# Kernel optimization log

Hardware: AMD Instinct MI355X
Metric: run time of the kernel (lower is better)

Reference implementation:

```python
import jax, jax.numpy as jnp
import numpy as np

BN_EPS = 1e-3
NUM_HEADS = 4
HEAD_CH = 16  # embed_channels // num_heads = 64 // 4


def _conv_bn(x, w, g, b, rm, rv, pad):
    # Conv2d (no bias) followed by eval-mode BatchNorm2d, activation=Identity.
    y = jax.lax.conv_general_dilated(
        x, w, window_strides=(1, 1), padding=[(pad, pad), (pad, pad)],
        dimension_numbers=("NCHW", "OIHW", "NCHW"))
    s = g * jax.lax.rsqrt(rv + BN_EPS)
    return y * s[None, :, None, None] + (b - rm * s)[None, :, None, None]


def setup_inputs() -> dict:
    key = jax.random.key(0)
    ks = jax.random.split(key, 16)
    B, Cin, H, W = 8, 128, 160, 160
    N, Cg, Ce, Co = 80, 512, 64, 128
    x = jax.random.normal(ks[0], (B, Cin, H, W), jnp.float32)
    guide = jax.random.normal(ks[1], (B, N, Cg), jnp.float32)
    # embed_conv (1x1) + BN params
    w_embed = jax.random.normal(ks[2], (Ce, Cin, 1, 1), jnp.float32) * 0.05
    g1 = jnp.ones((Ce,), jnp.float32)
    b1 = jnp.zeros((Ce,), jnp.float32)
    rm1 = jax.random.normal(ks[3], (Ce,), jnp.float32) * 0.1
    rv1 = jax.random.uniform(ks[4], (Ce,), jnp.float32) + 0.5
    # guide_fc
    Wg = jax.random.normal(ks[5], (Ce, Cg), jnp.float32) * 0.02
    bg = jnp.zeros((Ce,), jnp.float32)
    # per-head bias
    attn_bias = jnp.zeros((NUM_HEADS,), jnp.float32)
    # project_conv (3x3) + BN params
    w_proj = jax.random.normal(ks[6], (Co, Cin, 3, 3), jnp.float32) * 0.02
    g2 = jnp.ones((Co,), jnp.float32)
    b2 = jnp.zeros((Co,), jnp.float32)
    rm2 = jax.random.normal(ks[7], (Co,), jnp.float32) * 0.1
    rv2 = jax.random.uniform(ks[8], (Co,), jnp.float32) + 0.5
    return {"x": x, "guide": guide, "w_embed": w_embed, "g1": g1, "b1": b1,
            "rm1": rm1, "rv1": rv1, "Wg": Wg, "bg": bg, "attn_bias": attn_bias,
            "w_proj": w_proj, "g2": g2, "b2": b2, "rm2": rm2, "rv2": rv2}


def reference(x, guide, w_embed, g1, b1, rm1, rv1, Wg, bg, attn_bias,
              w_proj, g2, b2, rm2, rv2):
    B, _, H, W = x.shape
    nh, hc = NUM_HEADS, HEAD_CH
    # guide_fc -> [B, N, nh, hc]
    g = (jnp.einsum("bnc,ec->bne", guide, Wg) + bg).reshape(B, -1, nh, hc)
    # embed_conv (1x1, BN, no act) -> [B, nh, hc, H, W]
    e = _conv_bn(x, w_embed, g1, b1, rm1, rv1, 0).reshape(B, nh, hc, H, W)
    # attn: dot over head channels, max over N guides, scale, bias, sigmoid
    aw = jnp.einsum("bmchw,bnmc->bmhwn", e, g)  # [B, nh, H, W, N]
    aw = jnp.max(aw, axis=-1) * (1.0 / np.sqrt(hc)) + attn_bias[None, :, None, None]
    aw = jax.nn.sigmoid(aw)  # scale == 1.0 (with_scale=False)
    # project_conv (3x3, BN, no act), gate per-head, merge heads
    xp = _conv_bn(x, w_proj, g2, b2, rm2, rv2, 1).reshape(B, nh, -1, H, W)
    return (xp * aw[:, :, None]).reshape(B, -1, H, W)
```

## Files before the change

kernel.cpp:

```cpp
#include <hip/hip_runtime.h>
#include <hip/hip_bf16.h>
#include <stdint.h>


typedef __attribute__((ext_vector_type(8))) short short8;
typedef __attribute__((ext_vector_type(4))) float f32x4;

#define PCH2 ((size_t)8 * 162 * 176 * 32)

__device__ __forceinline__ unsigned short f2bf(float f) {
  unsigned int u = __float_as_uint(f);
  u += 0x7fff + ((u >> 16) & 1);
  return (unsigned short)(u >> 16);
}

__device__ __forceinline__ short8 zero8() {
  short8 z = {0,0,0,0,0,0,0,0};
  return z;
}

__global__ __launch_bounds__(192) void k_prep_x(const float* __restrict__ x,
                                                unsigned short* __restrict__ P2) {
  int b = blockIdx.x / 162, hp = blockIdx.x % 162;
  int wp = threadIdx.x;
  if (wp >= 176) return;
  size_t pix = (((size_t)b * 162 + hp) * 176 + wp) * 32;
  bool interior = (hp >= 1) && (hp <= 160) && (wp >= 8) && (wp < 168);
  if (!interior) {
#pragma unroll
    for (int cs = 0; cs < 4; ++cs)
#pragma unroll
      for (int s = 0; s < 4; ++s)
        *(short8*)(&P2[(size_t)cs * PCH2 + pix + s * 8]) = zero8();
    return;
  }
  int h = hp - 1, w = wp - 8;
  const float* xb = x + (size_t)b * 128 * 25600 + h * 160 + w;
  for (int cs = 0; cs < 4; ++cs) {
#pragma unroll
    for (int s = 0; s < 4; ++s) {
      short8 v;
#pragma unroll
      for (int j = 0; j < 8; ++j) {
        float f = xb[(size_t)(cs * 32 + s * 8 + j) * 25600];
        v[j] = (short)f2bf(f);
      }
      *(short8*)(&P2[(size_t)cs * PCH2 + pix + s * 8]) = v;
    }
  }
}

__global__ __launch_bounds__(256) void k_prep_misc(
    const float* __restrict__ w_embed, const float* __restrict__ w_proj,
    const float* __restrict__ g2, const float* __restrict__ b2,
    const float* __restrict__ rm2, const float* __restrict__ rv2,
    unsigned short* __restrict__ W1t, unsigned short* __restrict__ Wpt,
    float* __restrict__ s2, float* __restrict__ t2) {
  int idx = blockIdx.x * 256 + threadIdx.x;
  if (idx < 8192) { W1t[idx] = f2bf(w_embed[idx]); return; }
  idx -= 8192;
  if (idx < 147456) {
    int cs = idx / 36864, r = idx - cs * 36864;
    int tap = r >> 12, r2 = r & 4095;
    int co = r2 >> 5, ci5 = r2 & 31;
    int ci = cs * 32 + ci5;
    Wpt[idx] = f2bf(w_proj[(co * 128 + ci) * 9 + tap]);
    return;
  }
  idx -= 147456;
  if (idx < 128) {
    float s = g2[idx] * rsqrtf(rv2[idx] + 1e-3f);
    s2[idx] = s;
    t2[idx] = b2[idx] - rm2[idx] * s;
  }
}

__global__ __launch_bounds__(64) void k_guide(
    const float* __restrict__ guide, const float* __restrict__ Wg,
    const float* __restrict__ bg, const float* __restrict__ g1,
    const float* __restrict__ b1, const float* __restrict__ rm1,
    const float* __restrict__ rv1, unsigned short* __restrict__ Gpad,
    float* __restrict__ Cst) {
  int b = blockIdx.x / 80, n = blockIdx.x % 80;
  __shared__ float gs[512];
  const float* gr = guide + ((size_t)b * 80 + n) * 512;
  for (int i = threadIdx.x; i < 512; i += 64) gs[i] = gr[i];
  __syncthreads();
  int ce = threadIdx.x;
  const float* wr = Wg + (size_t)ce * 512;
  float acc = 0.f;
  for (int k = 0; k < 512; k += 4)
    acc += gs[k] * wr[k] + gs[k + 1] * wr[k + 1] + gs[k + 2] * wr[k + 2] +
           gs[k + 3] * wr[k + 3];
  float raw = acc + bg[ce];
  float s1 = g1[ce] * rsqrtf(rv1[ce] + 1e-3f);
  float t1 = b1[ce] - rm1[ce] * s1;
  int head = ce >> 4, c = ce & 15;
  size_t gp = (((size_t)b * 4 + head) * 80 + n) * 32;
  Gpad[gp + c] = f2bf(raw * s1);
  Gpad[gp + 16 + c] = 0;
  float cp = raw * t1;
  cp += __shfl_xor(cp, 1);
  cp += __shfl_xor(cp, 2);
  cp += __shfl_xor(cp, 4);
  cp += __shfl_xor(cp, 8);
  if (c == 0) Cst[((size_t)b * 4 + head) * 80 + n] = cp;
}

__global__ __launch_bounds__(256, 4) void k_attn(
    const unsigned short* __restrict__ P2, const unsigned short* __restrict__ W1t,
    const unsigned short* __restrict__ Gpad, const float* __restrict__ Cst,
    const float* __restrict__ attn_bias, float* __restrict__ aw) {
  __shared__ unsigned short E[16384];
  int b = blockIdx.x & 7;
  int px0 = (blockIdx.x >> 3) * 256;
  int tid = threadIdx.x, lane = tid & 63, wv = tid >> 6;
  int l15 = lane & 15, l4 = lane >> 4;

  f32x4 acc[4][4];
#pragma unroll
  for (int mt = 0; mt < 4; ++mt)
#pragma unroll
    for (int nt = 0; nt < 4; ++nt) acc[mt][nt] = (f32x4){0.f, 0.f, 0.f, 0.f};

  size_t Ab[4];
#pragma unroll
  for (int mt = 0; mt < 4; ++mt) {
    int px = px0 + wv * 64 + mt * 16 + l15;
    int h = px / 160, w = px - h * 160;
    Ab[mt] = (((size_t)b * 162 + h + 1) * 176 + (w + 8)) * 32;
  }
#pragma unroll
  for (int kc = 0; kc < 4; ++kc) {
    short8 A[4], Bf[4];
#pragma unroll
    for (int mt = 0; mt < 4; ++mt)
      A[mt] = *(const short8*)(P2 + (size_t)kc * PCH2 + Ab[mt] + l4 * 8);
#pragma unroll
    for (int nt = 0; nt < 4; ++nt)
      Bf[nt] = *(const short8*)(W1t + (nt * 16 + l15) * 128 + kc * 32 + l4 * 8);
#pragma unroll
    for (int mt = 0; mt < 4; ++mt)
#pragma unroll
      for (int nt = 0; nt < 4; ++nt)
        acc[mt][nt] = __builtin_amdgcn_mfma_f32_16x16x32_bf16(A[mt], Bf[nt],
                                                              acc[mt][nt], 0, 0, 0);
  }
#pragma unroll
  for (int mt = 0; mt < 4; ++mt)
#pragma unroll
    for (int nt = 0; nt < 4; ++nt)
#pragma unroll
      for (int r = 0; r < 4; ++r) {
        int pxl = wv * 64 + mt * 16 + l4 * 4 + r;
        int slot = (nt * 2 + (l15 >> 3)) ^ (pxl & 7);
        E[pxl * 64 + slot * 8 + (l15 & 7)] = f2bf(acc[mt][nt][r]);
      }
  __syncthreads();

  const f32x4 zf = (f32x4){0.f, 0.f, 0.f, 0.f};
#pragma unroll
  for (int head = 0; head < 4; ++head) {
    short8 Ga[5];
    f32x4 cst[5];
#pragma unroll
    for (int m5 = 0; m5 < 5; ++m5) {
      Ga[m5] = *(const short8*)(Gpad + (((size_t)b * 4 + head) * 80 + m5 * 16 + l15) * 32 + l4 * 8);
      cst[m5] = *(const f32x4*)(Cst + ((size_t)b * 4 + head) * 80 + m5 * 16 + l4 * 4);
    }
    float bias = attn_bias[head];
#pragma unroll
    for (int nt = 0; nt < 4; ++nt) {
      int pxl = wv * 64 + nt * 16 + l15;
      int rslot = (head * 2 + (l4 & 1)) ^ (pxl & 7);
      short8 Bf = *(const short8*)(&E[pxl * 64 + rslot * 8]);
      float mx = -3.0e38f;
#pragma unroll
      for (int m5 = 0; m5 < 5; ++m5) {
        f32x4 s = __builtin_amdgcn_mfma_f32_16x16x32_bf16(Ga[m5], Bf, zf, 0, 0, 0);
#pragma unroll
        for (int r = 0; r < 4; ++r) mx = fmaxf(mx, s[r] + cst[m5][r]);
      }
      mx = fmaxf(mx, __shfl_xor(mx, 16));
      mx = fmaxf(mx, __shfl_xor(mx, 32));
      if (lane < 16) {
        float v = 1.f / (1.f + __expf(-(mx * 0.25f + bias)));
        aw[((size_t)b * 4 + head) * 25600 + px0 + wv * 64 + nt * 16 + lane] = v;
      }
    }
  }
}

__global__ __launch_bounds__(256, 3) void k_conv(
    const unsigned short* __restrict__ P2, const unsigned short* __restrict__ Wpt,
    const float* __restrict__ s2, const float* __restrict__ t2,
    const float* __restrict__ aw, float* __restrict__ out) {
  __shared__ unsigned short XA[2][7680];
  __shared__ unsigned short XB[2][4096];
  int b = blockIdx.x & 7, r2b = blockIdx.x >> 3;
  int ht = r2b / 5, wt = r2b % 5;
  int h0 = ht * 4, w0 = wt * 32;
  int tid = threadIdx.x, lane = tid & 63, wv = tid >> 6;
  int l15 = lane & 15, l4 = lane >> 4;
  int mh = wv >> 1, nh = wv & 1;

  size_t aoff[4];
  bool aval[4];
#pragma unroll
  for (int i = 0; i < 4; ++i) {
    int c = i * 256 + tid;
    aval[i] = (c < 960);
    int cc = aval[i] ? c : 0;
    int row = cc / 160, rem = cc - row * 160;
    int px = rem >> 2, sp = rem & 3;
    int s = sp ^ ((px >> 1) & 3);
    aoff[i] = (((size_t)b * 162 + h0 + row) * 176 + (w0 + 7 + px)) * 32 + s * 8;
  }
  int boff[2];
#pragma unroll
  for (int i = 0; i < 2; ++i) {
    int c = i * 256 + tid;
    int co = c >> 2, sp = c & 3;
    boff[i] = co * 32 + (sp ^ ((co >> 1) & 3)) * 8;
  }
  int abase[2][3];
#pragma unroll
  for (int wh = 0; wh < 2; ++wh)
#pragma unroll
    for (int kx = 0; kx < 3; ++kx) {
      int px = wh * 16 + l15 + kx;
      abase[wh][kx] = px * 4 + (l4 ^ ((px >> 1) & 3));
    }
  int bchunk[4];
#pragma unroll
  for (int nt = 0; nt < 4; ++nt) {
    int co = nh * 64 + nt * 16 + l15;
    bchunk[nt] = co * 4 + (l4 ^ ((co >> 1) & 3));
  }

  f32x4 acc[4][4];
#pragma unroll
  for (int j = 0; j < 4; ++j)
#pragma unroll
    for (int nt = 0; nt < 4; ++nt) acc[j][nt] = (f32x4){0.f, 0.f, 0.f, 0.f};

  short8 areg[4], breg[2];
#pragma unroll
  for (int i = 0; i < 4; ++i)
    if (aval[i]) areg[i] = *(const short8*)(P2 + aoff[i]);
#pragma unroll
  for (int i = 0; i < 2; ++i) breg[i] = *(const short8*)(Wpt + boff[i]);
#pragma unroll
  for (int i = 0; i < 4; ++i)
    if (aval[i]) *(short8*)(&XA[0][(i * 256 + tid) * 8]) = areg[i];
#pragma unroll
  for (int i = 0; i < 2; ++i) *(short8*)(&XB[0][(i * 256 + tid) * 8]) = breg[i];
  __syncthreads();

  for (int cs = 0; cs < 4; ++cs) {
#pragma unroll
    for (int tap = 0; tap < 9; ++tap) {
      int t = cs * 9 + tap;
      int ky = tap / 3, kx = tap - ky * 3;
      if (tap == 0 && cs < 3) {
#pragma unroll
        for (int i = 0; i < 4; ++i)
          if (aval[i]) areg[i] = *(const short8*)(P2 + (size_t)(cs + 1) * PCH2 + aoff[i]);
      }
      if (t < 35) {
#pragma unroll
        for (int i = 0; i < 2; ++i)
          breg[i] = *(const short8*)(Wpt + (size_t)(t + 1) * 4096 + boff[i]);
      }
      short8 A[4], Bf[4];
#pragma unroll
      for (int j = 0; j < 4; ++j) {
        int row = mh * 2 + (j >> 1) + ky;
        A[j] = *(const short8*)(&XA[cs & 1][(row * 160 + abase[j & 1][kx]) * 8]);
      }
#pragma unroll
      for (int nt = 0; nt < 4; ++nt)
        Bf[nt] = *(const short8*)(&XB[t & 1][bchunk[nt] * 8]);
#pragma unroll
      for (int j = 0; j < 4; ++j)
#pragma unroll
        for (int nt = 0; nt < 4; ++nt)
          acc[j][nt] = __builtin_amdgcn_mfma_f32_16x16x32_bf16(A[j], Bf[nt],
                                                               acc[j][nt], 0, 0, 0);
      if (t < 35) {
#pragma unroll
        for (int i = 0; i < 2; ++i)
          *(short8*)(&XB[(t + 1) & 1][(i * 256 + tid) * 8]) = breg[i];
      }
      if (tap == 8 && cs < 3) {
#pragma unroll
        for (int i = 0; i < 4; ++i)
          if (aval[i]) *(short8*)(&XA[(cs + 1) & 1][(i * 256 + tid) * 8]) = areg[i];
      }
      if (t < 35) __syncthreads();
    }
  }

  float s2v[4], t2v[4];
#pragma unroll
  for (int nt = 0; nt < 4; ++nt) {
    int co = nh * 64 + nt * 16 + l15;
    s2v[nt] = s2[co];
    t2v[nt] = t2[co];
  }
#pragma unroll
  for (int j = 0; j < 4; ++j) {
    int hl = mh * 2 + (j >> 1), wh = j & 1;
    int h = h0 + hl, wbase = w0 + wh * 16 + l4 * 4;
    f32x4 aw0 = *(const f32x4*)(aw + (size_t)(b * 4 + nh * 2) * 25600 + h * 160 + wbase);
    f32x4 aw1 = *(const f32x4*)(aw + (size_t)(b * 4 + nh * 2 + 1) * 25600 + h * 160 + wbase);
#pragma unroll
    for (int nt = 0; nt < 4; ++nt) {
      int co = nh * 64 + nt * 16 + l15;
      f32x4 g = (nt < 2) ? aw0 : aw1;
      f32x4 o;
#pragma unroll
      for (int r = 0; r < 4; ++r) o[r] = (acc[j][nt][r] * s2v[nt] + t2v[nt]) * g[r];
      *(f32x4*)(out + (size_t)(b * 128 + co) * 25600 + h * 160 + wbase) = o;
    }
  }
}

extern "C" void kernel_launch(void* const* d_in, const int* in_sizes, int n_in,
                              void* d_out, int out_size, void* d_ws, size_t ws_size,
                              hipStream_t stream) {
  (void)in_sizes; (void)n_in; (void)out_size; (void)ws_size;
  const float* x         = (const float*)d_in[0];
  const float* guide     = (const float*)d_in[1];
  const float* w_embed   = (const float*)d_in[2];
  const float* g1        = (const float*)d_in[3];
  const float* b1        = (const float*)d_in[4];
  const float* rm1       = (const float*)d_in[5];
  const float* rv1       = (const float*)d_in[6];
  const float* Wg        = (const float*)d_in[7];
  const float* bg        = (const float*)d_in[8];
  const float* attn_bias = (const float*)d_in[9];
  const float* w_proj    = (const float*)d_in[10];
  const float* g2        = (const float*)d_in[11];
  const float* b2        = (const float*)d_in[12];
  const float* rm2       = (const float*)d_in[13];
  const float* rv2       = (const float*)d_in[14];
  float* out = (float*)d_out;

  char* ws = (char*)d_ws;
  unsigned short* P2   = (unsigned short*)(ws);
  unsigned short* W1t  = (unsigned short*)(ws + 58392576);
  unsigned short* Wpt  = (unsigned short*)(ws + 58408960);
  unsigned short* Gpad = (unsigned short*)(ws + 58703872);
  float* Cst           = (float*)(ws + 58867712);
  float* s2            = (float*)(ws + 58877952);
  float* t2            = (float*)(ws + 58878464);
  float* aw            = (float*)(ws + 58878976);

  k_prep_x<<<8 * 162, 192, 0, stream>>>(x, P2);
  k_prep_misc<<<609, 256, 0, stream>>>(w_embed, w_proj, g2, b2, rm2, rv2, W1t, Wpt, s2, t2);
  k_guide<<<640, 64, 0, stream>>>(guide, Wg, bg, g1, b1, rm1, rv1, Gpad, Cst);
  k_attn<<<800, 256, 0, stream>>>(P2, W1t, Gpad, Cst, attn_bias, aw);
  k_conv<<<1600, 256, 0, stream>>>(P2, Wpt, s2, t2, aw, out);
}
```

Before: 165.8 us.

## Fuse attention-gate computation into the 3x3 conv kernel and register-buffer weights

Merges the separate attention kernel into the conv kernel. The 1x1 embed GEMM reuses the centre-tap A fragments already staged in LDS, the embeddings are written into the freed XA buffer, and the per-pixel sigmoid gate is computed and kept in shared memory, so the aw round trip through global memory and one launch are gone. Conv weights are now read straight from global memory into a 3-deep register ring instead of being staged through LDS, which removes the per-tap barriers. The cost is higher register pressure (launch bounds lowered to 2 waves per SIMD), more global weight traffic per block, and some leftover dead variables.

```diff
diff --git a/kernel.cpp b/kernel.cpp
--- a/kernel.cpp
+++ b/kernel.cpp
@@ -107,96 +107,14 @@
   if (c == 0) Cst[((size_t)b * 4 + head) * 80 + n] = cp;
 }
 
-__global__ __launch_bounds__(256, 4) void k_attn(
+__global__ __launch_bounds__(256, 2) void k_mega(
     const unsigned short* __restrict__ P2, const unsigned short* __restrict__ W1t,
-    const unsigned short* __restrict__ Gpad, const float* __restrict__ Cst,
-    const float* __restrict__ attn_bias, float* __restrict__ aw) {
-  __shared__ unsigned short E[16384];
-  int b = blockIdx.x & 7;
-  int px0 = (blockIdx.x >> 3) * 256;
-  int tid = threadIdx.x, lane = tid & 63, wv = tid >> 6;
-  int l15 = lane & 15, l4 = lane >> 4;
-
-  f32x4 acc[4][4];
-#pragma unroll
-  for (int mt = 0; mt < 4; ++mt)
-#pragma unroll
-    for (int nt = 0; nt < 4; ++nt) acc[mt][nt] = (f32x4){0.f, 0.f, 0.f, 0.f};
-
-  size_t Ab[4];
-#pragma unroll
-  for (int mt = 0; mt < 4; ++mt) {
-    int px = px0 + wv * 64 + mt * 16 + l15;
-    int h = px / 160, w = px - h * 160;
-    Ab[mt] = (((size_t)b * 162 + h + 1) * 176 + (w + 8)) * 32;
-  }
-#pragma unroll
-  for (int kc = 0; kc < 4; ++kc) {
-    short8 A[4], Bf[4];
-#pragma unroll
-    for (int mt = 0; mt < 4; ++mt)
-      A[mt] = *(const short8*)(P2 + (size_t)kc * PCH2 + Ab[mt] + l4 * 8);
-#pragma unroll
-    for (int nt = 0; nt < 4; ++nt)
-      Bf[nt] = *(const short8*)(W1t + (nt * 16 + l15) * 128 + kc * 32 + l4 * 8);
-#pragma unroll
-    for (int mt = 0; mt < 4; ++mt)
-#pragma unroll
-      for (int nt = 0; nt < 4; ++nt)
-        acc[mt][nt] = __builtin_amdgcn_mfma_f32_16x16x32_bf16(A[mt], Bf[nt],
-                                                              acc[mt][nt], 0, 0, 0);
-  }
-#pragma unroll
-  for (int mt = 0; mt < 4; ++mt)
-#pragma unroll
-    for (int nt = 0; nt < 4; ++nt)
-#pragma unroll
-      for (int r = 0; r < 4; ++r) {
-        int pxl = wv * 64 + mt * 16 + l4 * 4 + r;
-        int slot = (nt * 2 + (l15 >> 3)) ^ (pxl & 7);
-        E[pxl * 64 + slot * 8 + (l15 & 7)] = f2bf(acc[mt][nt][r]);
-      }
-  __syncthreads();
-
-  const f32x4 zf = (f32x4){0.f, 0.f, 0.f, 0.f};
-#pragma unroll
-  for (int head = 0; head < 4; ++head) {
-    short8 Ga[5];
-    f32x4 cst[5];
-#pragma unroll
-    for (int m5 = 0; m5 < 5; ++m5) {
-      Ga[m5] = *(const short8*)(Gpad + (((size_t)b * 4 + head) * 80 + m5 * 16 + l15) * 32 + l4 * 8);
-      cst[m5] = *(const f32x4*)(Cst + ((size_t)b * 4 + head) * 80 + m5 * 16 + l4 * 4);
-    }
-    float bias = attn_bias[head];
-#pragma unroll
-    for (int nt = 0; nt < 4; ++nt) {
-      int pxl = wv * 64 + nt * 16 + l15;
-      int rslot = (head * 2 + (l4 & 1)) ^ (pxl & 7);
-      short8 Bf = *(const short8*)(&E[pxl * 64 + rslot * 8]);
-      float mx = -3.0e38f;
-#pragma unroll
-      for (int m5 = 0; m5 < 5; ++m5) {
-        f32x4 s = __builtin_amdgcn_mfma_f32_16x16x32_bf16(Ga[m5], Bf, zf, 0, 0, 0);
-#pragma unroll
-        for (int r = 0; r < 4; ++r) mx = fmaxf(mx, s[r] + cst[m5][r]);
-      }
-      mx = fmaxf(mx, __shfl_xor(mx, 16));
-      mx = fmaxf(mx, __shfl_xor(mx, 32));
-      if (lane < 16) {
-        float v = 1.f / (1.f + __expf(-(mx * 0.25f + bias)));
-        aw[((size_t)b * 4 + head) * 25600 + px0 + wv * 64 + nt * 16 + lane] = v;
-      }
-    }
-  }
-}
-
-__global__ __launch_bounds__(256, 3) void k_conv(
-    const unsigned short* __restrict__ P2, const unsigned short* __restrict__ Wpt,
+    const unsigned short* __restrict__ Wpt, const unsigned short* __restrict__ Gpad,
+    const float* __restrict__ Cst, const float* __restrict__ attn_bias,
     const float* __restrict__ s2, const float* __restrict__ t2,
-    const float* __restrict__ aw, float* __restrict__ out) {
+    float* __restrict__ out) {
   __shared__ unsigned short XA[2][7680];
-  __shared__ unsigned short XB[2][4096];
+  __shared__ float AWL[4][2][64];
   int b = blockIdx.x & 7, r2b = blockIdx.x >> 3;
   int ht = r2b / 5, wt = r2b % 5;
   int h0 = ht * 4, w0 = wt * 32;
@@ -216,13 +134,6 @@
     int s = sp ^ ((px >> 1) & 3);
     aoff[i] = (((size_t)b * 162 + h0 + row) * 176 + (w0 + 7 + px)) * 32 + s * 8;
   }
-  int boff[2];
-#pragma unroll
-  for (int i = 0; i < 2; ++i) {
-    int c = i * 256 + tid;
-    int co = c >> 2, sp = c & 3;
-    boff[i] = co * 32 + (sp ^ ((co >> 1) & 3)) * 8;
-  }
   int abase[2][3];
 #pragma unroll
   for (int wh = 0; wh < 2; ++wh)
@@ -231,73 +142,130 @@
       int px = wh * 16 + l15 + kx;
       abase[wh][kx] = px * 4 + (l4 ^ ((px >> 1) & 3));
     }
-  int bchunk[4];
-#pragma unroll
-  for (int nt = 0; nt < 4; ++nt) {
-    int co = nh * 64 + nt * 16 + l15;
-    bchunk[nt] = co * 4 + (l4 ^ ((co >> 1) & 3));
-  }
-
-  f32x4 acc[4][4];
-#pragma unroll
-  for (int j = 0; j < 4; ++j)
+  int bfo = (nh * 64 + l15 * 1 * 16 % 16, 0);
+  int bco = (nh * 64 + l15) * 0;
+  int boff[4];
+#pragma unroll
+  for (int nt = 0; nt < 4; ++nt) boff[nt] = (nh * 64 + nt * 16 + l15) * 32 + l4 * 8;
+
+  f32x4 acc[4][4], accE[4][2];
+#pragma unroll
+  for (int j = 0; j < 4; ++j) {
 #pragma unroll
     for (int nt = 0; nt < 4; ++nt) acc[j][nt] = (f32x4){0.f, 0.f, 0.f, 0.f};
-
-  short8 areg[4], breg[2];
+#pragma unroll
+    for (int ne = 0; ne < 2; ++ne) accE[j][ne] = (f32x4){0.f, 0.f, 0.f, 0.f};
+  }
+
+  short8 areg[4];
 #pragma unroll
   for (int i = 0; i < 4; ++i)
     if (aval[i]) areg[i] = *(const short8*)(P2 + aoff[i]);
 #pragma unroll
-  for (int i = 0; i < 2; ++i) breg[i] = *(const short8*)(Wpt + boff[i]);
-#pragma unroll
   for (int i = 0; i < 4; ++i)
     if (aval[i]) *(short8*)(&XA[0][(i * 256 + tid) * 8]) = areg[i];
-#pragma unroll
-  for (int i = 0; i < 2; ++i) *(short8*)(&XB[0][(i * 256 + tid) * 8]) = breg[i];
+
+  short8 Bbuf[3][4];
+#pragma unroll
+  for (int nt = 0; nt < 4; ++nt) {
+    Bbuf[0][nt] = *(const short8*)(Wpt + boff[nt]);
+    Bbuf[1][nt] = *(const short8*)(Wpt + 4096 + boff[nt]);
+  }
   __syncthreads();
 
+#pragma unroll
   for (int cs = 0; cs < 4; ++cs) {
+    if (cs < 3) {
+#pragma unroll
+      for (int i = 0; i < 4; ++i)
+        if (aval[i]) areg[i] = *(const short8*)(P2 + (size_t)(cs + 1) * PCH2 + aoff[i]);
+    }
 #pragma unroll
     for (int tap = 0; tap < 9; ++tap) {
-      int t = cs * 9 + tap;
+      const int t = cs * 9 + tap;
+      if (t + 2 < 36) {
+#pragma unroll
+        for (int nt = 0; nt < 4; ++nt)
+          Bbuf[(t + 2) % 3][nt] =
+              *(const short8*)(Wpt + (size_t)(t + 2) * 4096 + boff[nt]);
+      }
       int ky = tap / 3, kx = tap - ky * 3;
-      if (tap == 0 && cs < 3) {
-#pragma unroll
-        for (int i = 0; i < 4; ++i)
-          if (aval[i]) areg[i] = *(const short8*)(P2 + (size_t)(cs + 1) * PCH2 + aoff[i]);
-      }
-      if (t < 35) {
-#pragma unroll
-        for (int i = 0; i < 2; ++i)
-          breg[i] = *(const short8*)(Wpt + (size_t)(t + 1) * 4096 + boff[i]);
-      }
-      short8 A[4], Bf[4];
+      short8 A[4];
 #pragma unroll
       for (int j = 0; j < 4; ++j) {
-        int row = mh * 2 + (j >> 1) + ky;
-        A[j] = *(const short8*)(&XA[cs & 1][(row * 160 + abase[j & 1][kx]) * 8]);
-      }
-#pragma unroll
-      for (int nt = 0; nt < 4; ++nt)
-        Bf[nt] = *(const short8*)(&XB[t & 1][bchunk[nt] * 8]);
+        int rr = mh * 2 + (j >> 1) + ky;
+        A[j] = *(const short8*)(&XA[cs & 1][(rr * 160 + abase[j & 1][kx]) * 8]);
+      }
+      if (tap == 4) {
+        short8 BE[2];
+#pragma unroll
+        for (int ne = 0; ne < 2; ++ne)
+          BE[ne] = *(const short8*)(W1t + (nh * 32 + ne * 16 + l15) * 128 +
+                                    cs * 32 + l4 * 8);
+#pragma unroll
+        for (int j = 0; j < 4; ++j)
+#pragma unroll
+          for (int ne = 0; ne < 2; ++ne)
+            accE[j][ne] = __builtin_amdgcn_mfma_f32_16x16x32_bf16(
+                A[j], BE[ne], accE[j][ne], 0, 0, 0);
+      }
 #pragma unroll
       for (int j = 0; j < 4; ++j)
 #pragma unroll
         for (int nt = 0; nt < 4; ++nt)
-          acc[j][nt] = __builtin_amdgcn_mfma_f32_16x16x32_bf16(A[j], Bf[nt],
-                                                               acc[j][nt], 0, 0, 0);
-      if (t < 35) {
-#pragma unroll
-        for (int i = 0; i < 2; ++i)
-          *(short8*)(&XB[(t + 1) & 1][(i * 256 + tid) * 8]) = breg[i];
-      }
-      if (tap == 8 && cs < 3) {
-#pragma unroll
-        for (int i = 0; i < 4; ++i)
-          if (aval[i]) *(short8*)(&XA[(cs + 1) & 1][(i * 256 + tid) * 8]) = areg[i];
-      }
-      if (t < 35) __syncthreads();
+          acc[j][nt] = __builtin_amdgcn_mfma_f32_16x16x32_bf16(
+              A[j], Bbuf[t % 3][nt], acc[j][nt], 0, 0, 0);
+    }
+    if (cs < 3) {
+#pragma unroll
+      for (int i = 0; i < 4; ++i)
+        if (aval[i]) *(short8*)(&XA[(cs + 1) & 1][(i * 256 + tid) * 8]) = areg[i];
+      __syncthreads();
+    }
+  }
+  __syncthreads();
+
+  unsigned short* E = &XA[0][0];
+#pragma unroll
+  for (int j = 0; j < 4; ++j)
+#pragma unroll
+    for (int ne = 0; ne < 2; ++ne)
+#pragma unroll
+      for (int r = 0; r < 4; ++r) {
+        int pxl = mh * 64 + (j >> 1) * 32 + (j & 1) * 16 + l4 * 4 + r;
+        int ce = nh * 32 + ne * 16 + l15;
+        int slot = (ce >> 3) ^ (pxl & 7);
+        E[pxl * 64 + slot * 8 + (ce & 7)] = f2bf(accE[j][ne][r]);
+      }
+  __syncthreads();
+
+  const f32x4 zf = (f32x4){0.f, 0.f, 0.f, 0.f};
+#pragma unroll
+  for (int hh = 0; hh < 2; ++hh) {
+    int head = nh * 2 + hh;
+    short8 Ga[5];
+    f32x4 cst[5];
+#pragma unroll
+    for (int m5 = 0; m5 < 5; ++m5) {
+      Ga[m5] = *(const short8*)(Gpad + (((size_t)b * 4 + head) * 80 + m5 * 16 + l15) * 32 + l4 * 8);
+      cst[m5] = *(const f32x4*)(Cst + ((size_t)b * 4 + head) * 80 + m5 * 16 + l4 * 4);
+    }
+    float bias = attn_bias[head];
+#pragma unroll
+    for (int nt = 0; nt < 4; ++nt) {
+      int pxl = mh * 64 + nt * 16 + l15;
+      int rslot = (head * 2 + (l4 & 1)) ^ (pxl & 7);
+      short8 Bf = *(const short8*)(E + pxl * 64 + rslot * 8);
+      float mx = -3.0e38f;
+#pragma unroll
+      for (int m5 = 0; m5 < 5; ++m5) {
+        f32x4 s = __builtin_amdgcn_mfma_f32_16x16x32_bf16(Ga[m5], Bf, zf, 0, 0, 0);
+#pragma unroll
+        for (int r = 0; r < 4; ++r) mx = fmaxf(mx, s[r] + cst[m5][r]);
+      }
+      mx = fmaxf(mx, __shfl_xor(mx, 16));
+      mx = fmaxf(mx, __shfl_xor(mx, 32));
+      if (lane < 16) AWL[wv][hh][nt * 16 + lane] = 1.f / (1.f + __expf(-(mx * 0.25f + bias)));
     }
   }
 
@@ -310,14 +278,15 @@
   }
 #pragma unroll
   for (int j = 0; j < 4; ++j) {
-    int hl = mh * 2 + (j >> 1), wh = j & 1;
-    int h = h0 + hl, wbase = w0 + wh * 16 + l4 * 4;
-    f32x4 aw0 = *(const f32x4*)(aw + (size_t)(b * 4 + nh * 2) * 25600 + h * 160 + wbase);
-    f32x4 aw1 = *(const f32x4*)(aw + (size_t)(b * 4 + nh * 2 + 1) * 25600 + h * 160 + wbase);
+    int h = h0 + mh * 2 + (j >> 1);
+    int wbase = w0 + (j & 1) * 16 + l4 * 4;
+    int pb = (j >> 1) * 32 + (j & 1) * 16 + l4 * 4;
+    f32x4 a0 = *(const f32x4*)(&AWL[wv][0][pb]);
+    f32x4 a1 = *(const f32x4*)(&AWL[wv][1][pb]);
 #pragma unroll
     for (int nt = 0; nt < 4; ++nt) {
       int co = nh * 64 + nt * 16 + l15;
-      f32x4 g = (nt < 2) ? aw0 : aw1;
+      f32x4 g = (nt >> 1) ? a1 : a0;
       f32x4 o;
 #pragma unroll
       for (int r = 0; r < 4; ++r) o[r] = (acc[j][nt][r] * s2v[nt] + t2v[nt]) * g[r];
@@ -355,11 +324,9 @@
   float* Cst           = (float*)(ws + 58867712);
   float* s2            = (float*)(ws + 58877952);
   float* t2            = (float*)(ws + 58878464);
-  float* aw            = (float*)(ws + 58878976);
 
   k_prep_x<<<8 * 162, 192, 0, stream>>>(x, P2);
   k_prep_misc<<<609, 256, 0, stream>>>(w_embed, w_proj, g2, b2, rm2, rv2, W1t, Wpt, s2, t2);
   k_guide<<<640, 64, 0, stream>>>(guide, Wg, bg, g1, b1, rm1, rv1, Gpad, Cst);
-  k_attn<<<800, 256, 0, stream>>>(P2, W1t, Gpad, Cst, attn_bias, aw);
-  k_conv<<<1600, 256, 0, stream>>>(P2, Wpt, s2, t2, aw, out);
-}
+  k_mega<<<1600, 256, 0, stream>>>(P2, W1t, Wpt, Gpad, Cst, attn_bias, s2, t2, out);
+}
```

Measured after the change: 162.3 us. 1.02x faster.
